# Optimization experiments

Hardware: AMD Instinct MI355X
Metric: run time of the kernel (lower is better)

Reference implementation:

```python
import jax, jax.numpy as jnp
import numpy as np

B, S, D = 4, 2048, 1024
H = 16
DH = D // H


def setup_inputs() -> dict:
    key = jax.random.key(0)
    ks = jax.random.split(key, 9)
    s = 0.02
    return {
        "x": jax.random.normal(ks[0], (B, S, D), dtype=jnp.float32),
        "Wq": jax.random.normal(ks[1], (D, D), dtype=jnp.float32) * s,
        "bq": jax.random.normal(ks[2], (D,), dtype=jnp.float32) * s,
        "Wk": jax.random.normal(ks[3], (D, D), dtype=jnp.float32) * s,
        "bk": jax.random.normal(ks[4], (D,), dtype=jnp.float32) * s,
        "Wv": jax.random.normal(ks[5], (D, D), dtype=jnp.float32) * s,
        "bv": jax.random.normal(ks[6], (D,), dtype=jnp.float32) * s,
        "Wo": jax.random.normal(ks[7], (D, D), dtype=jnp.float32) * s,
        "bo": jax.random.normal(ks[8], (D,), dtype=jnp.float32) * s,
    }


def _split_heads(t):
    # [B,S,D] -> [B,H,S,DH]
    b, s, d = t.shape
    return t.reshape(b, s, H, DH).transpose(0, 2, 1, 3)


def reference(x, Wq, bq, Wk, bk, Wv, bv, Wo, bo):
    q = _split_heads(x @ Wq.T + bq)
    k = _split_heads(x @ Wk.T + bk)
    v = _split_heads(x @ Wv.T + bv)
    scale = 1.0 / np.sqrt(DH).astype(np.float32)
    scores = jnp.einsum("bhqd,bhkd->bhqk", q, k) * scale  # [B,H,S,S]
    s = scores.shape[-2]
    causal = jnp.tril(jnp.ones((s, s), dtype=bool))
    scores = jnp.where(causal[None, None], scores, -jnp.inf)
    probs = jax.nn.softmax(scores, axis=-1)
    out = jnp.einsum("bhqk,bhkd->bhqd", probs, v)  # [B,H,S,DH]
    out = out.transpose(0, 2, 1, 3).reshape(x.shape[0], s, D)
    return out @ Wo.T + bo
```

## Files before the change

kernel.cpp:

```cpp
#include <hip/hip_runtime.h>
#include <hip/hip_bf16.h>
#include <cstdint>
#include <cstddef>


typedef unsigned short u16;
typedef __bf16 bf16x8 __attribute__((ext_vector_type(8)));
typedef float  f32x4  __attribute__((ext_vector_type(4)));

__device__ __forceinline__ u16 f2bf(float f) {
  unsigned u = __float_as_uint(f);
  unsigned r = u + 0x7fffu + ((u >> 16) & 1u);
  return (u16)(r >> 16);
}

__device__ __forceinline__ void llds16(const u16* g, u16* l) {
  __builtin_amdgcn_global_load_lds(
      (const __attribute__((address_space(1))) void*)g,
      (__attribute__((address_space(3))) void*)l, 16, 0, 0);
}

__global__ void cast_bf16_kernel(const float* __restrict__ in, u16* __restrict__ out, int n4) {
  int i = blockIdx.x * blockDim.x + threadIdx.x;
  if (i >= n4) return;
  float4 f = ((const float4*)in)[i];
  ushort4 u;
  u.x = f2bf(f.x); u.y = f2bf(f.y); u.z = f2bf(f.z); u.w = f2bf(f.w);
  ((ushort4*)out)[i] = u;
}

__global__ void cast4_kernel(const float* __restrict__ a, const float* __restrict__ b,
                             const float* __restrict__ c, const float* __restrict__ d,
                             u16* __restrict__ oa, u16* __restrict__ ob,
                             u16* __restrict__ oc, u16* __restrict__ od, int n4) {
  const int w = blockIdx.y;
  const float* src = (w == 0) ? a : (w == 1) ? b : (w == 2) ? c : d;
  u16* dst = (w == 0) ? oa : (w == 1) ? ob : (w == 2) ? oc : od;
  int i = blockIdx.x * blockDim.x + threadIdx.x;
  if (i >= n4) return;
  float4 f = ((const float4*)src)[i];
  ushort4 u;
  u.x = f2bf(f.x); u.y = f2bf(f.y); u.z = f2bf(f.z); u.w = f2bf(f.w);
  ((ushort4*)dst)[i] = u;
}

__global__ __launch_bounds__(512) void gemm_qkv_256(
    const u16* __restrict__ A, const u16* __restrict__ Bw,
    const float* __restrict__ b0, const float* __restrict__ b1, const float* __restrict__ b2,
    u16* __restrict__ qkv_out)
{
  __shared__ u16 lds[57344];

  const int tid = threadIdx.x;
  const int lane = tid & 63;
  const int wave = tid >> 6;

  const int bid = (int)blockIdx.x;
  const int xcd = bid & 7;
  const int idx = bid >> 3;
  const int mt = (xcd << 2) | (idx & 3);
  const int nt = idx >> 2;
  const int m0 = mt << 8;
  const int n0 = nt * 192;

  const int warp_m = wave >> 2;
  const int warp_n = wave & 3;
  const int wm = warp_m << 7;
  const int wn = warp_n * 48;
  const int fr = lane & 15;
  const int g  = lane >> 4;

  const int srow = tid >> 3;
  const int schk = ((tid & 7) ^ (srow & 7)) << 3;
  const u16* pA = A  + (size_t)(m0 + srow) * 1024 + schk;
  const u16* pB = Bw + (size_t)(n0 + srow) * 1024 + schk;

  const int rsw0 = ((g    ) ^ (fr & 7)) << 3;
  const int rsw1 = ((g ^ 4) ^ (fr & 7)) << 3;

  const u16* Ab0 = lds + (size_t)(wm + fr) * 64;
  const u16* Bb0 = lds + 16384 + (size_t)(wn + fr) * 64;
  const u16* Ab1 = Ab0 + 28672;
  const u16* Bb1 = Bb0 + 28672;

  f32x4 acc[8][3];
  const f32x4 zero = {0.f, 0.f, 0.f, 0.f};
#pragma unroll
  for (int i = 0; i < 8; i++)
#pragma unroll
    for (int j = 0; j < 3; j++) acc[i][j] = zero;

  bf16x8 a_[4][2];
  bf16x8 b_[3][2];

  auto stageA = [&](int kt, int buf, int half) {
    const u16* src = pA + (size_t)half * 131072 + (kt << 6);
    u16* dst = lds + buf * 28672 + half * 8192 + tid * 8;
    llds16(src, dst);
    llds16(src + 65536, dst + 4096);
  };
  auto stageB0 = [&](int kt, int buf) {
    const u16* src = pB + (kt << 6);
    u16* dst = lds + buf * 28672 + 16384 + tid * 8;
    llds16(src, dst);
    llds16(src + 65536, dst + 4096);
  };
  auto stageB1 = [&](int kt, int buf) {
    const u16* src = pB + 131072 + (kt << 6);
    u16* dst = lds + buf * 28672 + 24576 + tid * 8;
    llds16(src, dst);
  };
  auto loadA4 = [&](const u16* Ab, int ib) {
#pragma unroll
    for (int ii = 0; ii < 4; ii++) {
      const u16* r = Ab + (ib + ii) * 1024;
      a_[ii][0] = *(const bf16x8*)(r + rsw0);
      a_[ii][1] = *(const bf16x8*)(r + rsw1);
    }
  };
  auto loadB = [&](const u16* Bb, int j0, int nj) {
#pragma unroll
    for (int jj = 0; jj < 3; jj++) {
      if (jj < nj) {
        const u16* r = Bb + (j0 + jj) * 1024;
        b_[j0 + jj][0] = *(const bf16x8*)(r + rsw0);
        b_[j0 + jj][1] = *(const bf16x8*)(r + rsw1);
      }
    }
  };
  auto mfmaQ = [&](int ib, int j0, int nj) {
    __builtin_amdgcn_s_setprio(1);
#pragma unroll
    for (int jj = 0; jj < 3; jj++) {
      if (jj < nj) {
#pragma unroll
        for (int ii = 0; ii < 4; ii++) {
          acc[ib+ii][j0+jj] = __builtin_amdgcn_mfma_f32_16x16x32_bf16(
              a_[ii][0], b_[j0+jj][0], acc[ib+ii][j0+jj], 0, 0, 0);
          acc[ib+ii][j0+jj] = __builtin_amdgcn_mfma_f32_16x16x32_bf16(
              a_[ii][1], b_[j0+jj][1], acc[ib+ii][j0+jj], 0, 0, 0);
        }
      }
    }
    __builtin_amdgcn_s_setprio(0);
  };

  stageA(0, 0, 0);
  stageA(0, 0, 1);
  stageB0(0, 0);
  stageB1(0, 0);
  stageA(1, 1, 0);
  asm volatile("s_waitcnt vmcnt(2)" ::: "memory");
  __builtin_amdgcn_s_barrier();

  const int NTI = 8;
  for (int t = 0; t < NTI; ++t) {
    const bool st = (t < NTI - 1);
    const int ka = 2 * t + 1;
    const int kb = 2 * t + 2;
    const int kc = 2 * t + 3;

    loadA4(Ab0, 0); loadB(Bb0, 0, 2);
    stageA(ka, 1, 1);
    __builtin_amdgcn_s_barrier();
    mfmaQ(0, 0, 2);
    __builtin_amdgcn_s_barrier();
    loadB(Bb0, 2, 1);
    stageB0(ka, 1);
    __builtin_amdgcn_s_barrier();
    mfmaQ(0, 2, 1);
    __builtin_amdgcn_s_barrier();
    loadA4(Ab0, 4);
    stageB1(ka, 1);
    __builtin_amdgcn_s_barrier();
    mfmaQ(4, 2, 1);
    __builtin_amdgcn_s_barrier();
    if (st) stageA(kb, 0, 0);
    __builtin_amdgcn_s_barrier();
    mfmaQ(4, 0, 2);
    if (st) { asm volatile("s_waitcnt vmcnt(2)" ::: "memory"); }
    else    { asm volatile("s_waitcnt vmcnt(0)" ::: "memory"); }
    __builtin_amdgcn_s_barrier();

    loadA4(Ab1, 0); loadB(Bb1, 0, 2);
    if (st) stageA(kb, 0, 1);
    __builtin_amdgcn_s_barrier();
    mfmaQ(0, 0, 2);
    __builtin_amdgcn_s_barrier();
    loadB(Bb1, 2, 1);
    if (st) stageB0(kb, 0);
    __builtin_amdgcn_s_barrier();
    mfmaQ(0, 2, 1);
    __builtin_amdgcn_s_barrier();
    loadA4(Ab1, 4);
    if (st) stageB1(kb, 0);
    __builtin_amdgcn_s_barrier();
    mfmaQ(4, 2, 1);
    __builtin_amdgcn_s_barrier();
    if (st) stageA(kc, 1, 0);
    __builtin_amdgcn_s_barrier();
    mfmaQ(4, 0, 2);
    if (st) { asm volatile("s_waitcnt vmcnt(2)" ::: "memory"); }
    __builtin_amdgcn_s_barrier();
  }

  __syncthreads();
  const int bI  = m0 >> 11;
  const int s0m = m0 & 2047;
#pragma unroll
  for (int j = 0; j < 3; j++) {
    const int ncol = n0 + wn + j * 16 + fr;
    const int which = ncol >> 10;
    const float bb = ((which == 0) ? b0 : (which == 1) ? b1 : b2)[ncol & 1023];
    const float post = (which == 0) ? 0.18033688011f : 1.0f;
    const int cl = wn + j * 16 + fr;
#pragma unroll
    for (int i = 0; i < 8; i++) {
#pragma unroll
      for (int r = 0; r < 4; r++) {
        const int row = wm + i * 16 + g * 4 + r;
        lds[row * 200 + cl] = f2bf((acc[i][j][r] + bb) * post);
      }
    }
  }
  __syncthreads();
  const int part = tid & 7;
#pragma unroll
  for (int p = 0; p < 12; p++) {
    const int hc = p >> 2;
    const int ml = ((p & 3) << 6) + (tid >> 3);
    const int ncol0 = n0 + hc * 64;
    const int which = ncol0 >> 10;
    const int h = (ncol0 >> 6) & 15;
    const bf16x8 v = *(const bf16x8*)(lds + ml * 200 + hc * 64 + part * 8);
    *(bf16x8*)(qkv_out + (size_t)which * 8388608 +
               ((size_t)(bI * 16 + h) * 2048 + s0m + ml) * 64 + part * 8) = v;
  }
}

__global__ __launch_bounds__(256) void gemm_bt(
    const u16* __restrict__ A, const u16* __restrict__ Bw,
    const float* __restrict__ b0, const float* __restrict__ b1, const float* __restrict__ b2,
    u16* __restrict__ qkv_out, float* __restrict__ flat_out,
    int K, int mode)
{
  __shared__ u16 As[128 * 32];
  __shared__ u16 Bs[128 * 32];

  const int tid = threadIdx.x;
  const int n0 = blockIdx.x * 128;
  const int m0 = blockIdx.y * 128;

  const int srow = tid >> 2;
  const int soff = (tid & 3) * 8;
  const u16* gA0 = A  + (size_t)(m0 + srow) * K + soff;
  const u16* gA1 = gA0 + (size_t)64 * K;
  const u16* gB0 = Bw + (size_t)(n0 + srow) * K + soff;
  const u16* gB1 = gB0 + (size_t)64 * K;
  u16* lA0 = As + tid * 8;
  u16* lA1 = As + 2048 + tid * 8;
  u16* lB0 = Bs + tid * 8;
  u16* lB1 = Bs + 2048 + tid * 8;

  const int lane = tid & 63;
  const int wave = tid >> 6;
  const int wm = (wave >> 1) * 64;
  const int wn = (wave & 1) * 64;
  const int fr = lane & 15;
  const int k8 = (lane >> 4) * 8;

  f32x4 zero = {0.f, 0.f, 0.f, 0.f};
  f32x4 acc[4][4];
#pragma unroll
  for (int i = 0; i < 4; i++)
#pragma unroll
    for (int j = 0; j < 4; j++) acc[i][j] = zero;

  for (int k0 = 0; k0 < K; k0 += 32) {
    llds16(gA0 + k0, lA0);
    llds16(gA1 + k0, lA1);
    llds16(gB0 + k0, lB0);
    llds16(gB1 + k0, lB1);
    __syncthreads();
    bf16x8 af[4], bfr[4];
#pragma unroll
    for (int i = 0; i < 4; i++)
      af[i] = *(const bf16x8*)(As + (wm + i * 16 + fr) * 32 + k8);
#pragma unroll
    for (int j = 0; j < 4; j++)
      bfr[j] = *(const bf16x8*)(Bs + (wn + j * 16 + fr) * 32 + k8);
#pragma unroll
    for (int i = 0; i < 4; i++)
#pragma unroll
      for (int j = 0; j < 4; j++)
        acc[i][j] = __builtin_amdgcn_mfma_f32_16x16x32_bf16(af[i], bfr[j], acc[i][j], 0, 0, 0);
    __syncthreads();
  }

  const int rbase = (lane >> 4) * 4;
  if (mode == 0) {
    const int which = n0 >> 10;
    const float* bias = (which == 0) ? b0 : ((which == 1) ? b1 : b2);
    const float post = (which == 0) ? 0.18033688011f : 1.0f;
    u16* outb = qkv_out + (size_t)which * 8388608;
#pragma unroll
    for (int j = 0; j < 4; j++) {
      const int nn = (n0 + wn + j * 16 + fr) & 1023;
      const float bb = bias[nn];
      const int h = nn >> 6, dh = nn & 63;
#pragma unroll
      for (int i = 0; i < 4; i++) {
#pragma unroll
        for (int r = 0; r < 4; r++) {
          const int m = m0 + wm + i * 16 + rbase + r;
          const int bI = m >> 11, s = m & 2047;
          outb[(((size_t)bI * 16 + h) * 2048 + s) * 64 + dh] = f2bf((acc[i][j][r] + bb) * post);
        }
      }
    }
  } else {
#pragma unroll
    for (int j = 0; j < 4; j++) {
      const int n = n0 + wn + j * 16 + fr;
      const float bb = b0[n];
#pragma unroll
      for (int i = 0; i < 4; i++) {
#pragma unroll
        for (int r = 0; r < 4; r++) {
          const int m = m0 + wm + i * 16 + rbase + r;
          flat_out[(size_t)m * 1024 + n] = acc[i][j][r] + bb;
        }
      }
    }
  }
}

__global__ __launch_bounds__(256) void transpose_v(const u16* __restrict__ V, u16* __restrict__ VT) {
  __shared__ u16 t_s[64 * 72];
  const int tid = threadIdx.x;
  const int st = blockIdx.x << 6;
  const int bh = blockIdx.y;
  const u16* src = V + ((size_t)bh * 2048 + st) * 64;
#pragma unroll
  for (int p = 0; p < 2; p++) {
    int i = p * 256 + tid;
    int row = i >> 3, ch = i & 7;
    bf16x8 v = *(const bf16x8*)(src + row * 64 + ch * 8);
    *(bf16x8*)(t_s + row * 72 + ch * 8) = v;
  }
  __syncthreads();
  u16* dst = VT + (size_t)bh * 131072 + st;
#pragma unroll
  for (int p = 0; p < 2; p++) {
    int i = p * 256 + tid;
    int dh = i >> 3, ch = i & 7;
    union { u16 s[8]; bf16x8 v; } u;
#pragma unroll
    for (int e = 0; e < 8; e++) u.s[e] = t_s[(ch * 8 + e) * 72 + dh];
    *(bf16x8*)(dst + (size_t)dh * 2048 + ch * 8) = u.v;
  }
}

__global__ __launch_bounds__(256, 2) void attn_fa(
    const u16* __restrict__ Qb, const u16* __restrict__ Kb,
    const u16* __restrict__ VT, u16* __restrict__ Ob)
{
  __shared__ u16 k_s[2 * 4096];
  __shared__ u16 v_s[2 * 4096];
  __shared__ u16 p_s[2 * 9216];
  __shared__ float l_s[256];

  const int tid = threadIdx.x;
  const int lane = tid & 63;
  const int wave = tid >> 6;

  const int c = (int)blockIdx.x;
  const int xcd = c & 7;
  const int rr_ = c >> 3;
  const int bh = xcd + ((rr_ >> 3) << 3);
  const int pr = rr_ & 7;
  const int qtA = pr;
  const int qtB = 15 - pr;

  const size_t head = (size_t)bh << 17;
  const int fr = lane & 15;
  const int g = lane >> 4;
  const int k8 = g << 3;
  const int q0A = qtA << 7;
  const int q0B = qtB << 7;
  const int wrow = wave << 5;

  bf16x8 aqA[2][2], aqB[2][2];
#pragma unroll
  for (int f = 0; f < 2; f++) {
    const u16* qpA = Qb + head + (size_t)(q0A + wrow + (f << 4) + fr) * 64;
    aqA[f][0] = *(const bf16x8*)(qpA + k8);
    aqA[f][1] = *(const bf16x8*)(qpA + 32 + k8);
    const u16* qpB = Qb + head + (size_t)(q0B + wrow + (f << 4) + fr) * 64;
    aqB[f][0] = *(const bf16x8*)(qpB + k8);
    aqB[f][1] = *(const bf16x8*)(qpB + 32 + k8);
  }

  const int r0 = tid >> 3, c0 = tid & 7;
  const int r1 = 32 + r0;
  const int koff0 = r0 * 64 + (((c0 ^ r0) & 7) << 3);
  const int koff1 = r1 * 64 + (((c0 ^ r1) & 7) << 3);
  const int voff0 = r0 * 2048 + (((c0 ^ r0) & 7) << 3);
  const int voff1 = r1 * 2048 + (((c0 ^ r1) & 7) << 3);
  int kaddr[4][2], vaddr[2][4];
#pragma unroll
  for (int j = 0; j < 4; j++) {
    const int kn = (j << 4) + fr;
    kaddr[j][0] = kn * 64 + (((g ^ kn) & 7) << 3);
    kaddr[j][1] = kn * 64 + ((((g + 4) ^ kn) & 7) << 3);
#pragma unroll
    for (int s2 = 0; s2 < 2; s2++)
      vaddr[s2][j] = kn * 64 + ((((s2 << 2) + g) ^ (kn & 7)) << 3);
  }
  u16* const prowA0 = p_s + (wrow + fr) * 72;
  u16* const prowA1 = p_s + (wrow + 16 + fr) * 72;
  u16* const prowB0 = p_s + 9216 + (wrow + fr) * 72;
  u16* const prowB1 = p_s + 9216 + (wrow + 16 + fr) * 72;
  const u16* Kbase = Kb + head;
  const u16* Vbase = VT + head;

  auto issueK = [&](int jt2, int buf) {
    const u16* Kt = Kbase + ((size_t)jt2 << 12);
    llds16(Kt + koff0, k_s + (buf << 12) + tid * 8);
    llds16(Kt + koff1, k_s + (buf << 12) + 2048 + tid * 8);
  };
  auto issueV = [&](int jt2, int buf) {
    const u16* Vt = Vbase + (jt2 << 6);
    llds16(Vt + voff0, v_s + (buf << 12) + tid * 8);
    llds16(Vt + voff1, v_s + (buf << 12) + 2048 + tid * 8);
  };

  f32x4 oA[2][4], oB[2][4];
  const f32x4 zero = {0.f, 0.f, 0.f, 0.f};
#pragma unroll
  for (int f = 0; f < 2; f++)
#pragma unroll
    for (int j = 0; j < 4; j++) { oA[f][j] = zero; oB[f][j] = zero; }
  float lA[2] = {0.f, 0.f}, lB[2] = {0.f, 0.f};

  const int jmax = 2 * qtB + 1;
  const int diagA = 2 * qtA + (wave >> 1);
  const int diagB = 2 * qtB + (wave >> 1);

  auto do_pv = [&](const u16* vs, f32x4 (&oacc)[2][4], const u16* p0r, const u16* p1r) {
#pragma unroll
    for (int s2 = 0; s2 < 2; s2++) {
      const bf16x8 ap0 = *(const bf16x8*)(p0r + (s2 << 5) + k8);
      const bf16x8 ap1 = *(const bf16x8*)(p1r + (s2 << 5) + k8);
#pragma unroll
      for (int j = 0; j < 4; j++) {
        const bf16x8 bv = *(const bf16x8*)(vs + vaddr[s2][j]);
        oacc[0][j] = __builtin_amdgcn_mfma_f32_16x16x32_bf16(ap0, bv, oacc[0][j], 0, 0, 0);
        oacc[1][j] = __builtin_amdgcn_mfma_f32_16x16x32_bf16(ap1, bv, oacc[1][j], 0, 0, 0);
      }
    }
  };

  auto do_s = [&](const u16* ks, int jt, bool dodiag, int q0t,
                  const bf16x8 (&aqt)[2][2], float (&lr)[2], u16* p0r, u16* p1r) {
    f32x4 s_acc[2][4];
#pragma unroll
    for (int f = 0; f < 2; f++)
#pragma unroll
      for (int j = 0; j < 4; j++) s_acc[f][j] = zero;
#pragma unroll
    for (int j = 0; j < 4; j++) {
      const bf16x8 ka0 = *(const bf16x8*)(ks + kaddr[j][0]);
      const bf16x8 ka1 = *(const bf16x8*)(ks + kaddr[j][1]);
      s_acc[0][j] = __builtin_amdgcn_mfma_f32_16x16x32_bf16(ka0, aqt[0][0], s_acc[0][j], 0, 0, 0);
      s_acc[0][j] = __builtin_amdgcn_mfma_f32_16x16x32_bf16(ka1, aqt[0][1], s_acc[0][j], 0, 0, 0);
      s_acc[1][j] = __builtin_amdgcn_mfma_f32_16x16x32_bf16(ka0, aqt[1][0], s_acc[1][j], 0, 0, 0);
      s_acc[1][j] = __builtin_amdgcn_mfma_f32_16x16x32_bf16(ka1, aqt[1][1], s_acc[1][j], 0, 0, 0);
    }
#pragma unroll
    for (int f = 0; f < 2; f++) {
      const int qa = q0t + wrow + (f << 4) + fr;
      u16* prow = (f == 0) ? p0r : p1r;
      if (dodiag) {
#pragma unroll
        for (int j = 0; j < 4; j++) {
          const int ka = (jt << 6) + (j << 4) + (g << 2);
          float p0 = (ka + 0 > qa) ? 0.f : __builtin_amdgcn_exp2f(s_acc[f][j][0]);
          float p1 = (ka + 1 > qa) ? 0.f : __builtin_amdgcn_exp2f(s_acc[f][j][1]);
          float p2 = (ka + 2 > qa) ? 0.f : __builtin_amdgcn_exp2f(s_acc[f][j][2]);
          float p3 = (ka + 3 > qa) ? 0.f : __builtin_amdgcn_exp2f(s_acc[f][j][3]);
          lr[f] += (p0 + p1) + (p2 + p3);
          union { __hip_bfloat162 h; unsigned u; } ca, cb;
          ca.h = __float22bfloat162_rn(make_float2(p0, p1));
          cb.h = __float22bfloat162_rn(make_float2(p2, p3));
          *(uint2*)(prow + (j << 4) + (g << 2)) = make_uint2(ca.u, cb.u);
        }
      } else {
#pragma unroll
        for (int j = 0; j < 4; j++) {
          float p0 = __builtin_amdgcn_exp2f(s_acc[f][j][0]);
          float p1 = __builtin_amdgcn_exp2f(s_acc[f][j][1]);
          float p2 = __builtin_amdgcn_exp2f(s_acc[f][j][2]);
          float p3 = __builtin_amdgcn_exp2f(s_acc[f][j][3]);
          lr[f] += (p0 + p1) + (p2 + p3);
          union { __hip_bfloat162 h; unsigned u; } ca, cb;
          ca.h = __float22bfloat162_rn(make_float2(p0, p1));
          cb.h = __float22bfloat162_rn(make_float2(p2, p3));
          *(uint2*)(prow + (j << 4) + (g << 2)) = make_uint2(ca.u, cb.u);
        }
      }
    }
  };

  issueK(0, 0);

  for (int jt = 0; jt <= jmax; jt++) {
    const int buf = jt & 1;
    __syncthreads();
    if (jt < jmax) issueK(jt + 1, buf ^ 1);
    issueV(jt, buf);
    if (jt > 0) {
      const u16* vprev = v_s + ((buf ^ 1) << 12);
      if (jt - 1 <= diagB) do_pv(vprev, oB, prowB0, prowB1);
      if (jt - 1 <= diagA) do_pv(vprev, oA, prowA0, prowA1);
    }
    if (jt <= diagB) do_s(k_s + (buf << 12), jt, jt == diagB, q0B, aqB, lB, prowB0, prowB1);
    if (jt <= diagA) do_s(k_s + (buf << 12), jt, jt == diagA, q0A, aqA, lA, prowA0, prowA1);
  }
  __syncthreads();
  if (diagB == jmax) do_pv(v_s + ((jmax & 1) << 12), oB, prowB0, prowB1);

#pragma unroll
  for (int f = 0; f < 2; f++) {
    float la = lA[f];
    la += __shfl_xor(la, 16);
    la += __shfl_xor(la, 32);
    if (g == 0) l_s[wrow + (f << 4) + fr] = la;
    float lb = lB[f];
    lb += __shfl_xor(lb, 16);
    lb += __shfl_xor(lb, 32);
    if (g == 0) l_s[128 + wrow + (f << 4) + fr] = lb;
  }
  const int b = bh >> 4, h = bh & 15;
#pragma unroll
  for (int f = 0; f < 2; f++) {
#pragma unroll
    for (int r = 0; r < 4; r++) {
      const int qloc = wrow + (f << 4) + (g << 2) + r;
      const float invA = 1.f / l_s[qloc];
      const float invB = 1.f / l_s[128 + qloc];
      const int qA_abs = q0A + qloc;
      const int qB_abs = q0B + qloc;
#pragma unroll
      for (int j = 0; j < 4; j++) {
        Ob[((size_t)b * 2048 + qA_abs) * 1024 + (h << 6) + (j << 4) + fr] =
            f2bf(oA[f][j][r] * invA);
        Ob[((size_t)b * 2048 + qB_abs) * 1024 + (h << 6) + (j << 4) + fr] =
            f2bf(oB[f][j][r] * invB);
      }
    }
  }
}

extern "C" void kernel_launch(void* const* d_in, const int* in_sizes, int n_in,
                              void* d_out, int out_size, void* d_ws, size_t ws_size,
                              hipStream_t stream) {
  const float* x  = (const float*)d_in[0];
  const float* Wq = (const float*)d_in[1];
  const float* bq = (const float*)d_in[2];
  const float* Wk = (const float*)d_in[3];
  const float* bk = (const float*)d_in[4];
  const float* Wv = (const float*)d_in[5];
  const float* bv = (const float*)d_in[6];
  const float* Wo = (const float*)d_in[7];
  const float* bo = (const float*)d_in[8];
  float* out = (float*)d_out;

  char* ws = (char*)d_ws;
  u16* xb    = (u16*)(ws);
  u16* vT    = (u16*)(ws);
  u16* wqkv  = (u16*)(ws + 16777216);
  u16* wo    = (u16*)(ws + 23068672);
  u16* qkv   = (u16*)(ws + 25165824);
  u16* attnb = (u16*)(ws + 75497472);

  cast_bf16_kernel<<<8192, 256, 0, stream>>>(x, xb, 2097152);
  cast4_kernel<<<dim3(1024, 4), 256, 0, stream>>>(
      Wq, Wk, Wv, Wo, wqkv, wqkv + 1048576, wqkv + 2097152, wo, 262144);

  gemm_qkv_256<<<dim3(512), 512, 0, stream>>>(xb, wqkv, bq, bk, bv, qkv);

  transpose_v<<<dim3(32, 64), 256, 0, stream>>>(qkv + 16777216, vT);

  attn_fa<<<dim3(512), 256, 0, stream>>>(qkv, qkv + 8388608, vT, attnb);

  gemm_bt<<<dim3(8, 64), 256, 0, stream>>>(attnb, wo, bo, bo, bo, nullptr, out, 1024, 1);
}
```

Measured before the change: 256.3 us.

## Split paired causal q-tiles into one tile per block, raise occupancy

Each attention block previously handled two mirrored causal query tiles (qt and 15-qt) to balance work, sharing each K/V tile load between them. Now each block handles a single 128-row query tile, the grid doubles to 1024, and blocks are ordered longest-first. LDS for P and row sums is halved, so launch bounds ask for 3 blocks per CU. This trades K/V reuse across the two tiles and the built-in load balancing for more parallelism and occupancy, and relies on the scheduler to balance the uneven causal work.

```diff
diff --git a/kernel.cpp b/kernel.cpp
--- a/kernel.cpp
+++ b/kernel.cpp
@@ -361,44 +361,34 @@
   }
 }
 
-__global__ __launch_bounds__(256, 2) void attn_fa(
+__global__ __launch_bounds__(256, 3) void attn_fa(
     const u16* __restrict__ Qb, const u16* __restrict__ Kb,
     const u16* __restrict__ VT, u16* __restrict__ Ob)
 {
   __shared__ u16 k_s[2 * 4096];
   __shared__ u16 v_s[2 * 4096];
-  __shared__ u16 p_s[2 * 9216];
-  __shared__ float l_s[256];
+  __shared__ u16 p_s[128 * 72];
+  __shared__ float l_s[128];
 
   const int tid = threadIdx.x;
   const int lane = tid & 63;
   const int wave = tid >> 6;
-
-  const int c = (int)blockIdx.x;
-  const int xcd = c & 7;
-  const int rr_ = c >> 3;
-  const int bh = xcd + ((rr_ >> 3) << 3);
-  const int pr = rr_ & 7;
-  const int qtA = pr;
-  const int qtB = 15 - pr;
-
+  const int bid = (int)blockIdx.x;
+  const int qt = 15 - (bid >> 6);
+  const int bh = (((bid >> 3) & 7) << 3) | (bid & 7);
   const size_t head = (size_t)bh << 17;
   const int fr = lane & 15;
   const int g = lane >> 4;
   const int k8 = g << 3;
-  const int q0A = qtA << 7;
-  const int q0B = qtB << 7;
+  const int q0 = qt << 7;
   const int wrow = wave << 5;
 
-  bf16x8 aqA[2][2], aqB[2][2];
+  bf16x8 aq[2][2];
 #pragma unroll
   for (int f = 0; f < 2; f++) {
-    const u16* qpA = Qb + head + (size_t)(q0A + wrow + (f << 4) + fr) * 64;
-    aqA[f][0] = *(const bf16x8*)(qpA + k8);
-    aqA[f][1] = *(const bf16x8*)(qpA + 32 + k8);
-    const u16* qpB = Qb + head + (size_t)(q0B + wrow + (f << 4) + fr) * 64;
-    aqB[f][0] = *(const bf16x8*)(qpB + k8);
-    aqB[f][1] = *(const bf16x8*)(qpB + 32 + k8);
+    const u16* qp = Qb + head + (size_t)(q0 + wrow + (f << 4) + fr) * 64;
+    aq[f][0] = *(const bf16x8*)(qp + k8);
+    aq[f][1] = *(const bf16x8*)(qp + 32 + k8);
   }
 
   const int r0 = tid >> 3, c0 = tid & 7;
@@ -417,10 +407,8 @@
     for (int s2 = 0; s2 < 2; s2++)
       vaddr[s2][j] = kn * 64 + ((((s2 << 2) + g) ^ (kn & 7)) << 3);
   }
-  u16* const prowA0 = p_s + (wrow + fr) * 72;
-  u16* const prowA1 = p_s + (wrow + 16 + fr) * 72;
-  u16* const prowB0 = p_s + 9216 + (wrow + fr) * 72;
-  u16* const prowB1 = p_s + 9216 + (wrow + 16 + fr) * 72;
+  u16* const prow0 = p_s + (wrow + fr) * 72;
+  u16* const prow1 = p_s + (wrow + 16 + fr) * 72;
   const u16* Kbase = Kb + head;
   const u16* Vbase = VT + head;
 
@@ -435,34 +423,32 @@
     llds16(Vt + voff1, v_s + (buf << 12) + 2048 + tid * 8);
   };
 
-  f32x4 oA[2][4], oB[2][4];
+  f32x4 o_acc[2][4];
   const f32x4 zero = {0.f, 0.f, 0.f, 0.f};
 #pragma unroll
   for (int f = 0; f < 2; f++)
 #pragma unroll
-    for (int j = 0; j < 4; j++) { oA[f][j] = zero; oB[f][j] = zero; }
-  float lA[2] = {0.f, 0.f}, lB[2] = {0.f, 0.f};
-
-  const int jmax = 2 * qtB + 1;
-  const int diagA = 2 * qtA + (wave >> 1);
-  const int diagB = 2 * qtB + (wave >> 1);
-
-  auto do_pv = [&](const u16* vs, f32x4 (&oacc)[2][4], const u16* p0r, const u16* p1r) {
+    for (int j = 0; j < 4; j++) o_acc[f][j] = zero;
+  float l_run[2] = {0.f, 0.f};
+
+  const int jmax = 2 * qt + 1;
+  const int jt_diag = 2 * qt + (wave >> 1);
+
+  auto do_pv = [&](const u16* vs) {
 #pragma unroll
     for (int s2 = 0; s2 < 2; s2++) {
-      const bf16x8 ap0 = *(const bf16x8*)(p0r + (s2 << 5) + k8);
-      const bf16x8 ap1 = *(const bf16x8*)(p1r + (s2 << 5) + k8);
+      const bf16x8 ap0 = *(const bf16x8*)(prow0 + (s2 << 5) + k8);
+      const bf16x8 ap1 = *(const bf16x8*)(prow1 + (s2 << 5) + k8);
 #pragma unroll
       for (int j = 0; j < 4; j++) {
         const bf16x8 bv = *(const bf16x8*)(vs + vaddr[s2][j]);
-        oacc[0][j] = __builtin_amdgcn_mfma_f32_16x16x32_bf16(ap0, bv, oacc[0][j], 0, 0, 0);
-        oacc[1][j] = __builtin_amdgcn_mfma_f32_16x16x32_bf16(ap1, bv, oacc[1][j], 0, 0, 0);
-      }
-    }
-  };
-
-  auto do_s = [&](const u16* ks, int jt, bool dodiag, int q0t,
-                  const bf16x8 (&aqt)[2][2], float (&lr)[2], u16* p0r, u16* p1r) {
+        o_acc[0][j] = __builtin_amdgcn_mfma_f32_16x16x32_bf16(ap0, bv, o_acc[0][j], 0, 0, 0);
+        o_acc[1][j] = __builtin_amdgcn_mfma_f32_16x16x32_bf16(ap1, bv, o_acc[1][j], 0, 0, 0);
+      }
+    }
+  };
+
+  auto do_s = [&](const u16* ks, bool dodiag, int jt) {
     f32x4 s_acc[2][4];
 #pragma unroll
     for (int f = 0; f < 2; f++)
@@ -472,24 +458,24 @@
     for (int j = 0; j < 4; j++) {
       const bf16x8 ka0 = *(const bf16x8*)(ks + kaddr[j][0]);
       const bf16x8 ka1 = *(const bf16x8*)(ks + kaddr[j][1]);
-      s_acc[0][j] = __builtin_amdgcn_mfma_f32_16x16x32_bf16(ka0, aqt[0][0], s_acc[0][j], 0, 0, 0);
-      s_acc[0][j] = __builtin_amdgcn_mfma_f32_16x16x32_bf16(ka1, aqt[0][1], s_acc[0][j], 0, 0, 0);
-      s_acc[1][j] = __builtin_amdgcn_mfma_f32_16x16x32_bf16(ka0, aqt[1][0], s_acc[1][j], 0, 0, 0);
-      s_acc[1][j] = __builtin_amdgcn_mfma_f32_16x16x32_bf16(ka1, aqt[1][1], s_acc[1][j], 0, 0, 0);
+      s_acc[0][j] = __builtin_amdgcn_mfma_f32_16x16x32_bf16(ka0, aq[0][0], s_acc[0][j], 0, 0, 0);
+      s_acc[0][j] = __builtin_amdgcn_mfma_f32_16x16x32_bf16(ka1, aq[0][1], s_acc[0][j], 0, 0, 0);
+      s_acc[1][j] = __builtin_amdgcn_mfma_f32_16x16x32_bf16(ka0, aq[1][0], s_acc[1][j], 0, 0, 0);
+      s_acc[1][j] = __builtin_amdgcn_mfma_f32_16x16x32_bf16(ka1, aq[1][1], s_acc[1][j], 0, 0, 0);
     }
 #pragma unroll
     for (int f = 0; f < 2; f++) {
-      const int qa = q0t + wrow + (f << 4) + fr;
-      u16* prow = (f == 0) ? p0r : p1r;
+      const int qa = q0 + wrow + (f << 4) + fr;
+      u16* prow = (f == 0) ? prow0 : prow1;
       if (dodiag) {
 #pragma unroll
         for (int j = 0; j < 4; j++) {
-          const int ka = (jt << 6) + (j << 4) + (g << 2);
-          float p0 = (ka + 0 > qa) ? 0.f : __builtin_amdgcn_exp2f(s_acc[f][j][0]);
-          float p1 = (ka + 1 > qa) ? 0.f : __builtin_amdgcn_exp2f(s_acc[f][j][1]);
-          float p2 = (ka + 2 > qa) ? 0.f : __builtin_amdgcn_exp2f(s_acc[f][j][2]);
-          float p3 = (ka + 3 > qa) ? 0.f : __builtin_amdgcn_exp2f(s_acc[f][j][3]);
-          lr[f] += (p0 + p1) + (p2 + p3);
+          const int kb = (jt << 6) + (j << 4) + (g << 2);
+          float p0 = (kb + 0 > qa) ? 0.f : __builtin_amdgcn_exp2f(s_acc[f][j][0]);
+          float p1 = (kb + 1 > qa) ? 0.f : __builtin_amdgcn_exp2f(s_acc[f][j][1]);
+          float p2 = (kb + 2 > qa) ? 0.f : __builtin_amdgcn_exp2f(s_acc[f][j][2]);
+          float p3 = (kb + 3 > qa) ? 0.f : __builtin_amdgcn_exp2f(s_acc[f][j][3]);
+          l_run[f] += (p0 + p1) + (p2 + p3);
           union { __hip_bfloat162 h; unsigned u; } ca, cb;
           ca.h = __float22bfloat162_rn(make_float2(p0, p1));
           cb.h = __float22bfloat162_rn(make_float2(p2, p3));
@@ -502,7 +488,7 @@
           float p1 = __builtin_amdgcn_exp2f(s_acc[f][j][1]);
           float p2 = __builtin_amdgcn_exp2f(s_acc[f][j][2]);
           float p3 = __builtin_amdgcn_exp2f(s_acc[f][j][3]);
-          lr[f] += (p0 + p1) + (p2 + p3);
+          l_run[f] += (p0 + p1) + (p2 + p3);
           union { __hip_bfloat162 h; unsigned u; } ca, cb;
           ca.h = __float22bfloat162_rn(make_float2(p0, p1));
           cb.h = __float22bfloat162_rn(make_float2(p2, p3));
@@ -515,31 +501,22 @@
   issueK(0, 0);
 
   for (int jt = 0; jt <= jmax; jt++) {
-    const int buf = jt & 1;
+    const int kb = jt & 1;
     __syncthreads();
-    if (jt < jmax) issueK(jt + 1, buf ^ 1);
-    issueV(jt, buf);
-    if (jt > 0) {
-      const u16* vprev = v_s + ((buf ^ 1) << 12);
-      if (jt - 1 <= diagB) do_pv(vprev, oB, prowB0, prowB1);
-      if (jt - 1 <= diagA) do_pv(vprev, oA, prowA0, prowA1);
-    }
-    if (jt <= diagB) do_s(k_s + (buf << 12), jt, jt == diagB, q0B, aqB, lB, prowB0, prowB1);
-    if (jt <= diagA) do_s(k_s + (buf << 12), jt, jt == diagA, q0A, aqA, lA, prowA0, prowA1);
+    if (jt < jmax) issueK(jt + 1, kb ^ 1);
+    issueV(jt, kb);
+    if (jt > 0 && jt - 1 <= jt_diag) do_pv(v_s + ((kb ^ 1) << 12));
+    if (jt <= jt_diag) do_s(k_s + (kb << 12), jt == jt_diag, jt);
   }
   __syncthreads();
-  if (diagB == jmax) do_pv(v_s + ((jmax & 1) << 12), oB, prowB0, prowB1);
+  if (jt_diag == jmax) do_pv(v_s + ((jmax & 1) << 12));
 
 #pragma unroll
   for (int f = 0; f < 2; f++) {
-    float la = lA[f];
-    la += __shfl_xor(la, 16);
-    la += __shfl_xor(la, 32);
-    if (g == 0) l_s[wrow + (f << 4) + fr] = la;
-    float lb = lB[f];
-    lb += __shfl_xor(lb, 16);
-    lb += __shfl_xor(lb, 32);
-    if (g == 0) l_s[128 + wrow + (f << 4) + fr] = lb;
+    float l = l_run[f];
+    l += __shfl_xor(l, 16);
+    l += __shfl_xor(l, 32);
+    if (g == 0) l_s[wrow + (f << 4) + fr] = l;
   }
   const int b = bh >> 4, h = bh & 15;
 #pragma unroll
@@ -547,17 +524,12 @@
 #pragma unroll
     for (int r = 0; r < 4; r++) {
       const int qloc = wrow + (f << 4) + (g << 2) + r;
-      const float invA = 1.f / l_s[qloc];
-      const float invB = 1.f / l_s[128 + qloc];
-      const int qA_abs = q0A + qloc;
-      const int qB_abs = q0B + qloc;
-#pragma unroll
-      for (int j = 0; j < 4; j++) {
-        Ob[((size_t)b * 2048 + qA_abs) * 1024 + (h << 6) + (j << 4) + fr] =
-            f2bf(oA[f][j][r] * invA);
-        Ob[((size_t)b * 2048 + qB_abs) * 1024 + (h << 6) + (j << 4) + fr] =
-            f2bf(oB[f][j][r] * invB);
-      }
+      const float inv = 1.f / l_s[qloc];
+      const int q_abs = q0 + qloc;
+#pragma unroll
+      for (int j = 0; j < 4; j++)
+        Ob[((size_t)b * 2048 + q_abs) * 1024 + (h << 6) + (j << 4) + fr] =
+            f2bf(o_acc[f][j][r] * inv);
     }
   }
 }
@@ -592,7 +564,7 @@
 
   transpose_v<<<dim3(32, 64), 256, 0, stream>>>(qkv + 16777216, vT);
 
-  attn_fa<<<dim3(512), 256, 0, stream>>>(qkv, qkv + 8388608, vT, attnb);
+  attn_fa<<<dim3(1024), 256, 0, stream>>>(qkv, qkv + 8388608, vT, attnb);
 
   gemm_bt<<<dim3(8, 64), 256, 0, stream>>>(attnb, wo, bo, bo, bo, nullptr, out, 1024, 1);
 }
```

Measured after the change: 247.7 us. 3.4% less time.
